# Performance work log

Measured on AMD Instinct MI355X. Metric: run time of the kernel, lower is better.

Reference implementation:

```python
import jax, jax.numpy as jnp
import numpy as np

DIM = 384
HEADS = 6
HIDDEN = int(DIM * 4.0)
EPS = 1e-6

def setup_inputs() -> dict:
    key = jax.random.key(0)
    ks = jax.random.split(key, 8)
    s = 0.02
    return {
        "x": jax.random.normal(ks[0], (4, 2048, DIM), dtype=jnp.float32),
        "w_qkv": jax.random.normal(ks[1], (DIM, 3 * DIM), dtype=jnp.float32) * s,
        "b_qkv": jnp.zeros((3 * DIM,), dtype=jnp.float32),
        "w_proj": jax.random.normal(ks[2], (DIM, DIM), dtype=jnp.float32) * s,
        "b_proj": jnp.zeros((DIM,), dtype=jnp.float32),
        "w_fc1": jax.random.normal(ks[3], (DIM, HIDDEN), dtype=jnp.float32) * s,
        "b_fc1": jnp.zeros((HIDDEN,), dtype=jnp.float32),
        "w_fc2": jax.random.normal(ks[4], (HIDDEN, DIM), dtype=jnp.float32) * s,
        "b_fc2": jnp.zeros((DIM,), dtype=jnp.float32),
        "g1": jnp.ones((DIM,), dtype=jnp.float32),
        "beta1": jnp.zeros((DIM,), dtype=jnp.float32),
        "g2": jnp.ones((DIM,), dtype=jnp.float32),
        "beta2": jnp.zeros((DIM,), dtype=jnp.float32),
    }

def _layernorm(x, g, b):
    mu = jnp.mean(x, axis=-1, keepdims=True)
    var = jnp.mean(jnp.square(x - mu), axis=-1, keepdims=True)
    return (x - mu) * jax.lax.rsqrt(var + EPS) * g + b

def _attention(x, w_qkv, b_qkv, w_proj, b_proj):
    B, N, C = x.shape
    H = HEADS
    Dh = C // H
    qkv = x @ w_qkv + b_qkv                      # [B,N,3C]
    qkv = qkv.reshape(B, N, 3, H, Dh)
    q = jnp.transpose(qkv[:, :, 0], (0, 2, 1, 3))  # [B,H,N,Dh]
    k = jnp.transpose(qkv[:, :, 1], (0, 2, 1, 3))
    v = jnp.transpose(qkv[:, :, 2], (0, 2, 1, 3))
    scale = Dh ** -0.5
    attn = jnp.einsum('bhnd,bhmd->bhnm', q, k) * scale
    attn = jax.nn.softmax(attn, axis=-1)
    out = jnp.einsum('bhnm,bhmd->bhnd', attn, v)
    out = jnp.transpose(out, (0, 2, 1, 3)).reshape(B, N, C)
    return out @ w_proj + b_proj

def _mlp(x, w_fc1, b_fc1, w_fc2, b_fc2):
    h = jax.nn.gelu(x @ w_fc1 + b_fc1, approximate=False)
    return h @ w_fc2 + b_fc2

def reference(x, w_qkv, b_qkv, w_proj, b_proj, w_fc1, b_fc1, w_fc2, b_fc2, g1, beta1, g2, beta2):
    x = x + _attention(_layernorm(x, g1, beta1), w_qkv, b_qkv, w_proj, b_proj)
    x = x + _mlp(_layernorm(x, g2, beta2), w_fc1, b_fc1, w_fc2, b_fc2)
    return x
```

## Files before the change

kernel.cpp:

```cpp
#include <hip/hip_runtime.h>
#include <hip/hip_bf16.h>

#define TOK 8192
#define CDIM 384
#define HEADS 6
#define DH 64
#define HID 1536
#define SEQ 2048

#define QSCALE 0.18033688011112042f

typedef short bf16x8 __attribute__((ext_vector_type(8)));
typedef short bf16x4 __attribute__((ext_vector_type(4)));
typedef float f32x4 __attribute__((ext_vector_type(4)));
typedef void __attribute__((address_space(1))) GV;
typedef void __attribute__((address_space(3))) SV;

__device__ __forceinline__ short f2bf(float f) {
    __hip_bfloat16 h = __float2bfloat16(f);
    return *reinterpret_cast<short*>(&h);
}

__device__ __forceinline__ int pack_bf2(float a, float b) {
    __hip_bfloat162 h2 = __float22bfloat162_rn(make_float2(a, b));
    int r;
    __builtin_memcpy(&r, &h2, 4);
    return r;
}

__device__ __forceinline__ void gl_lds16(const short* g, short* lds) {
    __builtin_amdgcn_global_load_lds((GV*)g, (SV*)lds, 16, 0, 0);
}

__device__ __forceinline__ float gelu_fast(float v) {
    const float A = 2.3022067f;
    const float B = 0.1029442f;
    const float u = v * (A + B * v * v);
    return v - v / (1.0f + exp2f(u));
}

__global__ __launch_bounds__(128) void ln_trans(const float* __restrict__ x,
                                                const float* __restrict__ g,
                                                const float* __restrict__ bta,
                                                short* __restrict__ y,
                                                const float* __restrict__ w_qkv,
                                                const float* __restrict__ w_proj,
                                                const float* __restrict__ w_fc1,
                                                const float* __restrict__ w_fc2,
                                                short* __restrict__ qkvT,
                                                short* __restrict__ projT,
                                                short* __restrict__ fc1T,
                                                short* __restrict__ fc2T) {
    if (blockIdx.x < TOK) {
        const int row = blockIdx.x;
        const float* xr = x + (size_t)row * CDIM;
        const int t = threadIdx.x;
        float v0 = xr[t], v1 = xr[t + 128], v2 = xr[t + 256];
        float s = v0 + v1 + v2;
        float ss = v0 * v0 + v1 * v1 + v2 * v2;
#pragma unroll
        for (int off = 1; off < 64; off <<= 1) {
            s += __shfl_xor(s, off);
            ss += __shfl_xor(ss, off);
        }
        __shared__ float sh[4];
        const int wv = t >> 6;
        if ((t & 63) == 0) { sh[wv] = s; sh[2 + wv] = ss; }
        __syncthreads();
        s = sh[0] + sh[1];
        ss = sh[2] + sh[3];
        const float mu = s * (1.0f / CDIM);
        const float var = ss * (1.0f / CDIM) - mu * mu;
        const float rs = rsqrtf(var + 1e-6f);
        short* yr = y + (size_t)row * CDIM;
        yr[t]       = f2bf((v0 - mu) * rs * g[t]       + bta[t]);
        yr[t + 128] = f2bf((v1 - mu) * rs * g[t + 128] + bta[t + 128]);
        yr[t + 256] = f2bf((v2 - mu) * rs * g[t + 256] + bta[t + 256]);
        return;
    }
    int b = blockIdx.x - TOK;
    const float* w; short* o; int K, N, nb;
    if (b < 432)       { w = w_qkv;  o = qkvT;  K = 384;  N = 1152; nb = 36; }
    else if (b < 576)  { b -= 432;  w = w_proj; o = projT; K = 384;  N = 384;  nb = 12; }
    else if (b < 1152) { b -= 576;  w = w_fc1;  o = fc1T;  K = 384;  N = 1536; nb = 48; }
    else               { b -= 1152; w = w_fc2;  o = fc2T;  K = 1536; N = 384;  nb = 12; }
    const int bx = (b % nb) * 32, by = (b / nb) * 32;
    __shared__ float t[32][33];
    const int tx = threadIdx.x & 31, ty = threadIdx.x >> 5;
#pragma unroll
    for (int i = 0; i < 8; ++i)
        t[ty + i * 4][tx] = w[(size_t)(by + ty + i * 4) * N + bx + tx];
    __syncthreads();
#pragma unroll
    for (int i = 0; i < 8; ++i)
        o[(size_t)(bx + ty + i * 4) * K + by + tx] = f2bf(t[tx][ty + i * 4]);
}

__global__ __launch_bounds__(128) void ln_kernel(const float* __restrict__ x,
                                                 const float* __restrict__ g,
                                                 const float* __restrict__ bta,
                                                 short* __restrict__ y) {
    const int row = blockIdx.x;
    const float* xr = x + (size_t)row * CDIM;
    const int t = threadIdx.x;
    float v0 = xr[t], v1 = xr[t + 128], v2 = xr[t + 256];
    float s = v0 + v1 + v2;
    float ss = v0 * v0 + v1 * v1 + v2 * v2;
#pragma unroll
    for (int off = 1; off < 64; off <<= 1) {
        s += __shfl_xor(s, off);
        ss += __shfl_xor(ss, off);
    }
    __shared__ float sh[4];
    const int wv = t >> 6;
    if ((t & 63) == 0) { sh[wv] = s; sh[2 + wv] = ss; }
    __syncthreads();
    s = sh[0] + sh[1];
    ss = sh[2] + sh[3];
    const float mu = s * (1.0f / CDIM);
    const float var = ss * (1.0f / CDIM) - mu * mu;
    const float rs = rsqrtf(var + 1e-6f);
    short* yr = y + (size_t)row * CDIM;
    yr[t]       = f2bf((v0 - mu) * rs * g[t]       + bta[t]);
    yr[t + 128] = f2bf((v1 - mu) * rs * g[t + 128] + bta[t + 128]);
    yr[t + 256] = f2bf((v2 - mu) * rs * g[t + 256] + bta[t + 256]);
}

template <int MODE, int MT>
__global__ __launch_bounds__(256) void mfma_gemm(const short* __restrict__ A,
                                                 const short* __restrict__ WT,
                                                 const float* __restrict__ bias,
                                                 const float* __restrict__ resid,
                                                 float* __restrict__ outF,
                                                 short* __restrict__ outB,
                                                 short* __restrict__ qb,
                                                 short* __restrict__ kb,
                                                 short* __restrict__ vtb,
                                                 int M, int N, int K) {
    constexpr int BN = (MT == 4) ? 128 : 64;
    constexpr int BM = (MT == 1) ? 64 : 128;
    __shared__ __align__(16) short As[BM * 64];
    __shared__ __align__(16) short Bs[BN * 64];

    const int tid  = threadIdx.x;
    const int w    = tid >> 6;
    const int lane = tid & 63;
    const int quad = lane >> 4;
    const int n15  = lane & 15;
    const int wr   = (MT == 4) ? (w >> 1) : w;
    const int wc   = (MT == 4) ? (w & 1) : 0;
    const int m0   = blockIdx.y * BM;
    const int n0   = blockIdx.x * BN;
    const int swz  = n15 & 7;

    f32x4 acc[MT][4];
#pragma unroll
    for (int i = 0; i < MT; ++i)
#pragma unroll
        for (int j = 0; j < 4; ++j) {
            acc[i][j][0] = 0; acc[i][j][1] = 0; acc[i][j][2] = 0; acc[i][j][3] = 0;
        }

    for (int k0 = 0; k0 < K; k0 += 64) {
        __syncthreads();
#pragma unroll
        for (int i = 0; i < BM / 32; ++i) {
            const int c = i * 256 + tid;
            const int r = c >> 3, p = c & 7;
            gl_lds16(A + (size_t)(m0 + r) * K + k0 + ((p ^ (r & 7)) * 8),
                     As + (i * 256 + w * 64) * 8);
        }
#pragma unroll
        for (int i = 0; i < BN / 32; ++i) {
            const int c = i * 256 + tid;
            const int r = c >> 3, p = c & 7;
            gl_lds16(WT + (size_t)(n0 + r) * K + k0 + ((p ^ (r & 7)) * 8),
                     Bs + (i * 256 + w * 64) * 8);
        }
        __syncthreads();

#pragma unroll
        for (int kk = 0; kk < 2; ++kk) {
            bf16x8 af[MT], bfr[4];
#pragma unroll
            for (int mt = 0; mt < MT; ++mt)
                af[mt] = *(const bf16x8*)&As[(wr * (MT * 16) + mt * 16 + n15) * 64 +
                                             (((kk * 4 + quad) ^ swz) * 8)];
#pragma unroll
            for (int nt = 0; nt < 4; ++nt)
                bfr[nt] = *(const bf16x8*)&Bs[(wc * 64 + nt * 16 + n15) * 64 +
                                              (((kk * 4 + quad) ^ swz) * 8)];
#pragma unroll
            for (int mt = 0; mt < MT; ++mt)
#pragma unroll
                for (int nt = 0; nt < 4; ++nt)
                    acc[mt][nt] = __builtin_amdgcn_mfma_f32_16x16x32_bf16(af[mt], bfr[nt], acc[mt][nt], 0, 0, 0);
        }
    }

#pragma unroll
    for (int nt = 0; nt < 4; ++nt) {
        const int col = n0 + wc * 64 + nt * 16 + n15;
        const float bv = bias[col];
        if constexpr (MODE == 2) {
            const int part = col / CDIM;
            const int rem  = col - part * CDIM;
            const int h    = rem >> 6;
            const int d    = rem & 63;
#pragma unroll
            for (int mt = 0; mt < MT; ++mt) {
                const int r0 = m0 + wr * (MT * 16) + mt * 16 + quad * 4;
                const int bi = r0 >> 11;
                const int n  = r0 & 2047;
                if (part == 2) {
                    short4 pkv;
                    pkv.x = f2bf(acc[mt][nt][0] + bv);
                    pkv.y = f2bf(acc[mt][nt][1] + bv);
                    pkv.z = f2bf(acc[mt][nt][2] + bv);
                    pkv.w = f2bf(acc[mt][nt][3] + bv);
                    *(short4*)&vtb[((size_t)(bi * HEADS + h) * DH + d) * SEQ + n] = pkv;
                } else {
                    short* dst = (part == 0 ? qb : kb) +
                                 ((size_t)(bi * HEADS + h) * SEQ + n) * DH + d;
#pragma unroll
                    for (int rr = 0; rr < 4; ++rr) {
                        float o = acc[mt][nt][rr] + bv;
                        if (part == 0) o *= QSCALE;
                        dst[(size_t)rr * DH] = f2bf(o);
                    }
                }
            }
        } else {
#pragma unroll
            for (int mt = 0; mt < MT; ++mt)
#pragma unroll
                for (int rr = 0; rr < 4; ++rr) {
                    const int r = m0 + wr * (MT * 16) + mt * 16 + quad * 4 + rr;
                    float o = acc[mt][nt][rr] + bv;
                    if constexpr (MODE == 1) {
                        outB[(size_t)r * N + col] = f2bf(gelu_fast(o));
                    } else {
                        if (resid) o += resid[(size_t)r * N + col];
                        outF[(size_t)r * N + col] = o;
                    }
                }
        }
    }
}

__global__ __launch_bounds__(256) void attn_mfma(const short* __restrict__ qb,
                                                 const short* __restrict__ kb,
                                                 const short* __restrict__ vtb,
                                                 short* __restrict__ outp) {
    __shared__ __align__(16) char smem[36864];
    short* Ql = (short*)smem;

    const int bid = blockIdx.x;
    const int x   = bid & 7;
    const int j   = bid >> 3;
    const int bh  = x * 3 + (j >> 6);
    const int qt  = j & 63;
    const int bi  = bh / HEADS;
    const int h   = bh - bi * HEADS;

    const int tid  = threadIdx.x;
    const int w    = tid >> 6;
    const int lane = tid & 63;
    const int quad = lane >> 4;
    const int n15  = lane & 15;
    const int swz  = n15 & 7;

    short* Kl  = (short*)(smem + 4096 + w * 8192);
    short* Vtl = (short*)(smem + 4096 + w * 8192 + 4096);

    const size_t headoff = (size_t)bh * SEQ * DH;

    {
        const short* qg = qb + headoff + (size_t)qt * 32 * DH;
        const int c = w * 64 + lane;
        const int r = c >> 3, p = c & 7;
        gl_lds16(qg + r * 64 + ((p ^ (r & 7)) * 8), Ql + (c - lane) * 8);
    }
    __syncthreads();

    bf16x8 qf[2][2];
#pragma unroll
    for (int mt = 0; mt < 2; ++mt) {
        qf[mt][0] = *(const bf16x8*)&Ql[(mt * 16 + n15) * 64 + ((quad ^ swz) * 8)];
        qf[mt][1] = *(const bf16x8*)&Ql[(mt * 16 + n15) * 64 + (((4 + quad) ^ swz) * 8)];
    }

    const int l3 = lane >> 3, l7 = lane & 7;
    const int l2 = lane >> 2, p4 = lane & 3;
    const short* kg = kb + headoff + l3 * 64 + ((l7 ^ l3) * 8) + (size_t)w * 32 * DH;
    const short* vg = vtb + (size_t)bh * DH * SEQ + (size_t)l2 * SEQ + ((p4 ^ (l2 & 3)) * 8) + w * 32;

    f32x4 O[2][4], O4[2];
#pragma unroll
    for (int mt = 0; mt < 2; ++mt) {
        O4[mt][0] = 0; O4[mt][1] = 0; O4[mt][2] = 0; O4[mt][3] = 0;
#pragma unroll
        for (int nt = 0; nt < 4; ++nt) {
            O[mt][nt][0] = 0; O[mt][nt][1] = 0; O[mt][nt][2] = 0; O[mt][nt][3] = 0;
        }
    }

    bf16x4 onesf;
    { const short one = 0x3F80; onesf[0] = one; onesf[1] = one; onesf[2] = one; onesf[3] = one; }

    for (int t = 0; t < SEQ / 128; ++t) {
#pragma unroll
        for (int i = 0; i < 4; ++i) {
            gl_lds16(kg + i * 512, Kl + i * 512);
            gl_lds16(vg + (size_t)i * 16 * SEQ, Vtl + i * 512);
        }
        kg += 128 * DH;
        vg += 128;
        __builtin_amdgcn_s_waitcnt(0x0F70);
        __builtin_amdgcn_wave_barrier();

#pragma unroll
        for (int nt = 0; nt < 2; ++nt) {
            f32x4 S[2];
#pragma unroll
            for (int mt = 0; mt < 2; ++mt) { S[mt][0] = 0; S[mt][1] = 0; S[mt][2] = 0; S[mt][3] = 0; }
#pragma unroll
            for (int kc = 0; kc < 2; ++kc) {
                const bf16x8 kf = *(const bf16x8*)&Kl[(nt * 16 + n15) * 64 + (((kc * 4 + quad) ^ swz) * 8)];
#pragma unroll
                for (int mt = 0; mt < 2; ++mt)
                    S[mt] = __builtin_amdgcn_mfma_f32_16x16x32_bf16(kf, qf[mt][kc], S[mt], 0, 0, 0);
            }
            bf16x4 af[2];
#pragma unroll
            for (int mt = 0; mt < 2; ++mt) {
                int pk[2];
                pk[0] = pack_bf2(exp2f(S[mt][0]), exp2f(S[mt][1]));
                pk[1] = pack_bf2(exp2f(S[mt][2]), exp2f(S[mt][3]));
                __builtin_memcpy(&af[mt], pk, 8);
            }
#pragma unroll
            for (int ntd = 0; ntd < 4; ++ntd) {
                const int row = ntd * 16 + n15;
                const int pchunk = (2 * nt + (quad >> 1)) ^ (row & 3);
                const bf16x4 vf = *(const bf16x4*)&Vtl[row * 32 + pchunk * 8 + (quad & 1) * 4];
#pragma unroll
                for (int mt = 0; mt < 2; ++mt)
                    O[mt][ntd] = __builtin_amdgcn_mfma_f32_16x16x16bf16_1k(af[mt], vf, O[mt][ntd], 0, 0, 0);
            }
#pragma unroll
            for (int mt = 0; mt < 2; ++mt)
                O4[mt] = __builtin_amdgcn_mfma_f32_16x16x16bf16_1k(af[mt], onesf, O4[mt], 0, 0, 0);
        }
    }

    __syncthreads();
    float* Obuf = (float*)smem;
    float* lbuf = (float*)(smem + 33280);
    float* myO = Obuf + w * 2080;
#pragma unroll
    for (int mt = 0; mt < 2; ++mt) {
#pragma unroll
        for (int ntd = 0; ntd < 4; ++ntd)
#pragma unroll
            for (int rr = 0; rr < 4; ++rr)
                myO[(mt * 16 + quad * 4 + rr) * 65 + ntd * 16 + n15] = O[mt][ntd][rr];
        if (n15 == 0)
#pragma unroll
            for (int rr = 0; rr < 4; ++rr)
                lbuf[w * 32 + mt * 16 + quad * 4 + rr] = O4[mt][rr];
    }
    __syncthreads();

    const int d = w * 16 + n15;
#pragma unroll
    for (int i = 0; i < 8; ++i) {
        const int q = quad * 8 + i;
        const float l = lbuf[q] + lbuf[32 + q] + lbuf[64 + q] + lbuf[96 + q];
        const float s = Obuf[q * 65 + d] + Obuf[2080 + q * 65 + d] +
                        Obuf[4160 + q * 65 + d] + Obuf[6240 + q * 65 + d];
        outp[(size_t)(bi * SEQ + qt * 32 + q) * CDIM + h * DH + d] = f2bf(s / l);
    }
}

extern "C" void kernel_launch(void* const* d_in, const int* in_sizes, int n_in,
                              void* d_out, int out_size, void* d_ws, size_t ws_size,
                              hipStream_t stream) {
    const float* x      = (const float*)d_in[0];
    const float* w_qkv  = (const float*)d_in[1];
    const float* b_qkv  = (const float*)d_in[2];
    const float* w_proj = (const float*)d_in[3];
    const float* b_proj = (const float*)d_in[4];
    const float* w_fc1  = (const float*)d_in[5];
    const float* b_fc1  = (const float*)d_in[6];
    const float* w_fc2  = (const float*)d_in[7];
    const float* b_fc2  = (const float*)d_in[8];
    const float* g1     = (const float*)d_in[9];
    const float* beta1  = (const float*)d_in[10];
    const float* g2     = (const float*)d_in[11];
    const float* beta2  = (const float*)d_in[12];
    float* out = (float*)d_out;

    short* qkvT = (short*)d_ws;
    short* projT = qkvT + 1152 * 384;
    short* fc1T  = projT + 384 * 384;
    short* fc2T  = fc1T + 1536 * 384;
    short* y     = fc2T + 384 * 1536;
    short* qb    = y + (size_t)TOK * 384;
    short* kb    = qb + (size_t)TOK * 384;
    short* vtb   = kb + (size_t)TOK * 384;
    short* attn  = vtb + (size_t)TOK * 384;
    short* hbuf  = attn + (size_t)TOK * 384;

    ln_trans<<<TOK + 1728, 128, 0, stream>>>(x, g1, beta1, y,
                                             w_qkv, w_proj, w_fc1, w_fc2,
                                             qkvT, projT, fc1T, fc2T);
    mfma_gemm<2, 4><<<dim3(1152 / 128, TOK / 128), 256, 0, stream>>>(
        y, qkvT, b_qkv, nullptr, nullptr, nullptr, qb, kb, vtb, TOK, 3 * CDIM, CDIM);
    attn_mfma<<<1536, 256, 0, stream>>>(qb, kb, vtb, attn);
    mfma_gemm<0, 1><<<dim3(CDIM / 64, TOK / 64), 256, 0, stream>>>(
        attn, projT, b_proj, x, out, nullptr, nullptr, nullptr, nullptr, TOK, CDIM, CDIM);
    ln_kernel<<<TOK, 128, 0, stream>>>(out, g2, beta2, y);
    mfma_gemm<1, 4><<<dim3(HID / 128, TOK / 128), 256, 0, stream>>>(
        y, fc1T, b_fc1, nullptr, nullptr, hbuf, nullptr, nullptr, nullptr, TOK, HID, CDIM);
    mfma_gemm<0, 1><<<dim3(CDIM / 64, TOK / 64), 256, 0, stream>>>(
        hbuf, fc2T, b_fc2, out, out, nullptr, nullptr, nullptr, nullptr, TOK, CDIM, HID);
}
```

Before: 241.8 us.

## Rewrite attention inner loop with 32x32 MFMA and direct register loads

The attention kernel switches from 16x16 MFMA tiles staged through LDS to 32x32x16 bf16 MFMAs fed by direct global-to-register loads of Q, K and V^T, with the loop fully unrolled. The softmax probabilities are reshuffled between lane halves with v_permlane32_swap, so the P operand is built without LDS. The row sum is now accumulated with scalar adds instead of an extra MFMA against a ones vector. This drops the LDS staging, the wait counts and the wave barriers in the loop, at the cost of more register pressure and uncoalesced global loads that rely on L1/L2 caching of K and V.

```diff
diff --git a/kernel.cpp b/kernel.cpp
--- a/kernel.cpp
+++ b/kernel.cpp
@@ -13,6 +13,7 @@
 typedef short bf16x8 __attribute__((ext_vector_type(8)));
 typedef short bf16x4 __attribute__((ext_vector_type(4)));
 typedef float f32x4 __attribute__((ext_vector_type(4)));
+typedef float f32x16 __attribute__((ext_vector_type(16)));
 typedef void __attribute__((address_space(1))) GV;
 typedef void __attribute__((address_space(3))) SV;
 
@@ -252,8 +253,7 @@
                                                  const short* __restrict__ kb,
                                                  const short* __restrict__ vtb,
                                                  short* __restrict__ outp) {
-    __shared__ __align__(16) char smem[36864];
-    short* Ql = (short*)smem;
+    __shared__ __align__(16) float smem[8448];
 
     const int bid = blockIdx.x;
     const int x   = bid & 7;
@@ -266,112 +266,84 @@
     const int tid  = threadIdx.x;
     const int w    = tid >> 6;
     const int lane = tid & 63;
+    const int l31  = lane & 31;
+    const int hi   = lane >> 5;
+
+    const size_t headoff = (size_t)bh * SEQ * DH;
+
+    bf16x8 qf[4];
+    {
+        const short* qg = qb + headoff + (size_t)(qt * 32 + l31) * DH + hi * 8;
+#pragma unroll
+        for (int kc = 0; kc < 4; ++kc)
+            qf[kc] = *(const bf16x8*)(qg + kc * 16);
+    }
+
+    const short* kgp = kb + headoff + (size_t)(w * 32 + l31) * DH + hi * 8;
+    const short* vgp = vtb + (size_t)bh * DH * SEQ + (size_t)l31 * SEQ + w * 32 + hi * 8;
+
+    f32x16 O0 = {}, O1 = {};
+    float lp = 0.0f;
+    const f32x16 Zc = {};
+
+#pragma unroll
+    for (int t = 0; t < SEQ / 128; ++t) {
+        const short* kg = kgp + (size_t)t * 128 * DH;
+        const short* vg = vgp + t * 128;
+        bf16x8 kf0 = *(const bf16x8*)(kg);
+        bf16x8 kf1 = *(const bf16x8*)(kg + 16);
+        bf16x8 kf2 = *(const bf16x8*)(kg + 32);
+        bf16x8 kf3 = *(const bf16x8*)(kg + 48);
+        bf16x8 v00 = *(const bf16x8*)(vg);
+        bf16x8 v01 = *(const bf16x8*)(vg + 16);
+        bf16x8 v10 = *(const bf16x8*)(vg + 65536);
+        bf16x8 v11 = *(const bf16x8*)(vg + 65536 + 16);
+
+        f32x16 S = __builtin_amdgcn_mfma_f32_32x32x16_bf16(kf0, qf[0], Zc, 0, 0, 0);
+        S = __builtin_amdgcn_mfma_f32_32x32x16_bf16(kf1, qf[1], S, 0, 0, 0);
+        S = __builtin_amdgcn_mfma_f32_32x32x16_bf16(kf2, qf[2], S, 0, 0, 0);
+        S = __builtin_amdgcn_mfma_f32_32x32x16_bf16(kf3, qf[3], S, 0, 0, 0);
+
+        float e[16];
+#pragma unroll
+        for (int r = 0; r < 16; ++r) e[r] = exp2f(S[r]);
+        lp += (((e[0] + e[1]) + (e[2] + e[3])) + ((e[4] + e[5]) + (e[6] + e[7]))) +
+              (((e[8] + e[9]) + (e[10] + e[11])) + ((e[12] + e[13]) + (e[14] + e[15])));
+
+        int p0 = pack_bf2(e[0], e[1]),  p1 = pack_bf2(e[2], e[3]);
+        int p2 = pack_bf2(e[4], e[5]),  p3 = pack_bf2(e[6], e[7]);
+        asm("v_permlane32_swap_b32 %0, %1" : "+v"(p0), "+v"(p2));
+        asm("v_permlane32_swap_b32 %0, %1" : "+v"(p1), "+v"(p3));
+        int p4 = pack_bf2(e[8], e[9]),  p5 = pack_bf2(e[10], e[11]);
+        int p6 = pack_bf2(e[12], e[13]), p7 = pack_bf2(e[14], e[15]);
+        asm("v_permlane32_swap_b32 %0, %1" : "+v"(p4), "+v"(p6));
+        asm("v_permlane32_swap_b32 %0, %1" : "+v"(p5), "+v"(p7));
+        bf16x8 pf0, pf1;
+        { int pw[4] = {p0, p1, p2, p3}; __builtin_memcpy(&pf0, pw, 16); }
+        { int pw[4] = {p4, p5, p6, p7}; __builtin_memcpy(&pf1, pw, 16); }
+
+        O0 = __builtin_amdgcn_mfma_f32_32x32x16_bf16(v00, pf0, O0, 0, 0, 0);
+        O0 = __builtin_amdgcn_mfma_f32_32x32x16_bf16(v01, pf1, O0, 0, 0, 0);
+        O1 = __builtin_amdgcn_mfma_f32_32x32x16_bf16(v10, pf0, O1, 0, 0, 0);
+        O1 = __builtin_amdgcn_mfma_f32_32x32x16_bf16(v11, pf1, O1, 0, 0, 0);
+    }
+
+    lp += __shfl_xor(lp, 32);
+
+    float* Obuf = smem;
+    float* lbuf = smem + 8320;
+    float* myO  = Obuf + w * 2080;
+#pragma unroll
+    for (int r = 0; r < 16; ++r) {
+        const int d0 = (r & 3) + 8 * (r >> 2) + 4 * hi;
+        myO[l31 * 65 + d0]      = O0[r];
+        myO[l31 * 65 + 32 + d0] = O1[r];
+    }
+    if (hi == 0) lbuf[w * 32 + l31] = lp;
+    __syncthreads();
+
     const int quad = lane >> 4;
     const int n15  = lane & 15;
-    const int swz  = n15 & 7;
-
-    short* Kl  = (short*)(smem + 4096 + w * 8192);
-    short* Vtl = (short*)(smem + 4096 + w * 8192 + 4096);
-
-    const size_t headoff = (size_t)bh * SEQ * DH;
-
-    {
-        const short* qg = qb + headoff + (size_t)qt * 32 * DH;
-        const int c = w * 64 + lane;
-        const int r = c >> 3, p = c & 7;
-        gl_lds16(qg + r * 64 + ((p ^ (r & 7)) * 8), Ql + (c - lane) * 8);
-    }
-    __syncthreads();
-
-    bf16x8 qf[2][2];
-#pragma unroll
-    for (int mt = 0; mt < 2; ++mt) {
-        qf[mt][0] = *(const bf16x8*)&Ql[(mt * 16 + n15) * 64 + ((quad ^ swz) * 8)];
-        qf[mt][1] = *(const bf16x8*)&Ql[(mt * 16 + n15) * 64 + (((4 + quad) ^ swz) * 8)];
-    }
-
-    const int l3 = lane >> 3, l7 = lane & 7;
-    const int l2 = lane >> 2, p4 = lane & 3;
-    const short* kg = kb + headoff + l3 * 64 + ((l7 ^ l3) * 8) + (size_t)w * 32 * DH;
-    const short* vg = vtb + (size_t)bh * DH * SEQ + (size_t)l2 * SEQ + ((p4 ^ (l2 & 3)) * 8) + w * 32;
-
-    f32x4 O[2][4], O4[2];
-#pragma unroll
-    for (int mt = 0; mt < 2; ++mt) {
-        O4[mt][0] = 0; O4[mt][1] = 0; O4[mt][2] = 0; O4[mt][3] = 0;
-#pragma unroll
-        for (int nt = 0; nt < 4; ++nt) {
-            O[mt][nt][0] = 0; O[mt][nt][1] = 0; O[mt][nt][2] = 0; O[mt][nt][3] = 0;
-        }
-    }
-
-    bf16x4 onesf;
-    { const short one = 0x3F80; onesf[0] = one; onesf[1] = one; onesf[2] = one; onesf[3] = one; }
-
-    for (int t = 0; t < SEQ / 128; ++t) {
-#pragma unroll
-        for (int i = 0; i < 4; ++i) {
-            gl_lds16(kg + i * 512, Kl + i * 512);
-            gl_lds16(vg + (size_t)i * 16 * SEQ, Vtl + i * 512);
-        }
-        kg += 128 * DH;
-        vg += 128;
-        __builtin_amdgcn_s_waitcnt(0x0F70);
-        __builtin_amdgcn_wave_barrier();
-
-#pragma unroll
-        for (int nt = 0; nt < 2; ++nt) {
-            f32x4 S[2];
-#pragma unroll
-            for (int mt = 0; mt < 2; ++mt) { S[mt][0] = 0; S[mt][1] = 0; S[mt][2] = 0; S[mt][3] = 0; }
-#pragma unroll
-            for (int kc = 0; kc < 2; ++kc) {
-                const bf16x8 kf = *(const bf16x8*)&Kl[(nt * 16 + n15) * 64 + (((kc * 4 + quad) ^ swz) * 8)];
-#pragma unroll
-                for (int mt = 0; mt < 2; ++mt)
-                    S[mt] = __builtin_amdgcn_mfma_f32_16x16x32_bf16(kf, qf[mt][kc], S[mt], 0, 0, 0);
-            }
-            bf16x4 af[2];
-#pragma unroll
-            for (int mt = 0; mt < 2; ++mt) {
-                int pk[2];
-                pk[0] = pack_bf2(exp2f(S[mt][0]), exp2f(S[mt][1]));
-                pk[1] = pack_bf2(exp2f(S[mt][2]), exp2f(S[mt][3]));
-                __builtin_memcpy(&af[mt], pk, 8);
-            }
-#pragma unroll
-            for (int ntd = 0; ntd < 4; ++ntd) {
-                const int row = ntd * 16 + n15;
-                const int pchunk = (2 * nt + (quad >> 1)) ^ (row & 3);
-                const bf16x4 vf = *(const bf16x4*)&Vtl[row * 32 + pchunk * 8 + (quad & 1) * 4];
-#pragma unroll
-                for (int mt = 0; mt < 2; ++mt)
-                    O[mt][ntd] = __builtin_amdgcn_mfma_f32_16x16x16bf16_1k(af[mt], vf, O[mt][ntd], 0, 0, 0);
-            }
-#pragma unroll
-            for (int mt = 0; mt < 2; ++mt)
-                O4[mt] = __builtin_amdgcn_mfma_f32_16x16x16bf16_1k(af[mt], onesf, O4[mt], 0, 0, 0);
-        }
-    }
-
-    __syncthreads();
-    float* Obuf = (float*)smem;
-    float* lbuf = (float*)(smem + 33280);
-    float* myO = Obuf + w * 2080;
-#pragma unroll
-    for (int mt = 0; mt < 2; ++mt) {
-#pragma unroll
-        for (int ntd = 0; ntd < 4; ++ntd)
-#pragma unroll
-            for (int rr = 0; rr < 4; ++rr)
-                myO[(mt * 16 + quad * 4 + rr) * 65 + ntd * 16 + n15] = O[mt][ntd][rr];
-        if (n15 == 0)
-#pragma unroll
-            for (int rr = 0; rr < 4; ++rr)
-                lbuf[w * 32 + mt * 16 + quad * 4 + rr] = O4[mt][rr];
-    }
-    __syncthreads();
-
     const int d = w * 16 + n15;
 #pragma unroll
     for (int i = 0; i < 8; ++i) {
```

Measured after the change: 272.4 us. 1.13x slower.
